# Kernel tuning notes

Hardware: AMD Instinct MI355X
Metric: run time of the kernel (lower is better)

The kernel has to match this reference:

```python
import jax, jax.numpy as jnp
import numpy as np

TIME_STEPS = 20
THRESHOLD = 1.0
DECAY = 0.9


def setup_inputs() -> dict:
    key = jax.random.key(0)
    x = jax.random.uniform(key, (64, 8192), dtype=jnp.float32)
    return {"x": x}


def reference(x):
    # LIF recurrence over TIME_STEPS: mem = decay*mem + x; spike = mem >= thr;
    # record (spike, mem); then mem -= spike*thr. Sequential -> lax.scan.
    thr = jnp.asarray(THRESHOLD, dtype=x.dtype)
    decay = jnp.asarray(DECAY, dtype=x.dtype)

    def step(mem, _):
        mem = decay * mem + x
        spikes = (mem >= thr).astype(x.dtype)
        mem_out = mem  # recorded before reset
        mem_next = mem - spikes * thr
        return mem_next, (spikes, mem_out)

    mem0 = jnp.zeros_like(x)
    _, (spike_trains, membrane_potentials) = jax.lax.scan(
        step, mem0, None, length=TIME_STEPS)
    # shapes: [T, batch, features]
    return spike_trains, membrane_potentials
```

## Files before the change

kernel.cpp:

```cpp
#include <hip/hip_runtime.h>


#define TSTEPS 20

typedef float v4f __attribute__((ext_vector_type(4)));

__global__ __launch_bounds__(256) void
TemporalEncoding_57672820850797_kernel(const v4f* __restrict__ x,
                                       float* __restrict__ out, int n4) {
    int i = blockIdx.x * blockDim.x + threadIdx.x;
    if (i >= n4) return;

    const v4f xv = __builtin_nontemporal_load(&x[i]);
    v4f* __restrict__ spikes = reinterpret_cast<v4f*>(out) + i;
    v4f* __restrict__ mems   = reinterpret_cast<v4f*>(out) + (size_t)TSTEPS * n4 + i;

    float m0 = 0.f, m1 = 0.f, m2 = 0.f, m3 = 0.f;

#pragma unroll
    for (int t = 0; t < TSTEPS; ++t) {
        m0 = __fadd_rn(__fmul_rn(0.9f, m0), xv.x);
        m1 = __fadd_rn(__fmul_rn(0.9f, m1), xv.y);
        m2 = __fadd_rn(__fmul_rn(0.9f, m2), xv.z);
        m3 = __fadd_rn(__fmul_rn(0.9f, m3), xv.w);

        float s0 = (m0 >= 1.0f) ? 1.0f : 0.0f;
        float s1 = (m1 >= 1.0f) ? 1.0f : 0.0f;
        float s2 = (m2 >= 1.0f) ? 1.0f : 0.0f;
        float s3 = (m3 >= 1.0f) ? 1.0f : 0.0f;

        v4f sv; sv.x = s0; sv.y = s1; sv.z = s2; sv.w = s3;
        v4f mv; mv.x = m0; mv.y = m1; mv.z = m2; mv.w = m3;
        __builtin_nontemporal_store(sv, spikes);
        __builtin_nontemporal_store(mv, mems);
        spikes += n4;
        mems   += n4;

        m0 -= s0;
        m1 -= s1;
        m2 -= s2;
        m3 -= s3;
    }
}

extern "C" void kernel_launch(void* const* d_in, const int* in_sizes, int n_in,
                              void* d_out, int out_size, void* d_ws, size_t ws_size,
                              hipStream_t stream) {
    const float* x = (const float*)d_in[0];
    float* out = (float*)d_out;
    const int n = in_sizes[0];
    const int n4 = n / 4;
    const int block = 256;
    const int grid = (n4 + block - 1) / block;
    TemporalEncoding_57672820850797_kernel<<<grid, block, 0, stream>>>(
        (const v4f*)x, out, n4);
}
```

Before: 90.29 us.

## Split output writes into contiguous per-block slabs with persistent grid-stride blocks

Replaces one-thread-per-element work (each thread writing 40 strided vectors across all time steps) with a persistent 512-block grid. Each work item covers one output type (spikes or membrane) and one group of 5 time steps, and recomputes the recurrence from zero up to that group. This makes each block write into one contiguous region of the output, which should improve DRAM write locality. The price is redundant recomputation of the recurrence and sizes hard-coded for this input shape. The load of x also changes from nontemporal to a normal load.

```diff
diff --git a/kernel.cpp b/kernel.cpp
--- a/kernel.cpp
+++ b/kernel.cpp
@@ -2,23 +2,19 @@
 
 
 #define TSTEPS 20
+#define TPER 5
+#define NGROUPS (TSTEPS / TPER)
+#define N4 131072
+#define CHUNKS 512
 
 typedef float v4f __attribute__((ext_vector_type(4)));
 
-__global__ __launch_bounds__(256) void
-TemporalEncoding_57672820850797_kernel(const v4f* __restrict__ x,
-                                       float* __restrict__ out, int n4) {
-    int i = blockIdx.x * blockDim.x + threadIdx.x;
-    if (i >= n4) return;
-
-    const v4f xv = __builtin_nontemporal_load(&x[i]);
-    v4f* __restrict__ spikes = reinterpret_cast<v4f*>(out) + i;
-    v4f* __restrict__ mems   = reinterpret_cast<v4f*>(out) + (size_t)TSTEPS * n4 + i;
-
+template <int TLO, bool SPIKES>
+__device__ __forceinline__ void run_store(const v4f xv, v4f* __restrict__ dst,
+                                          int n4) {
     float m0 = 0.f, m1 = 0.f, m2 = 0.f, m3 = 0.f;
-
 #pragma unroll
-    for (int t = 0; t < TSTEPS; ++t) {
+    for (int t = 0; t < TLO + TPER; ++t) {
         m0 = __fadd_rn(__fmul_rn(0.9f, m0), xv.x);
         m1 = __fadd_rn(__fmul_rn(0.9f, m1), xv.y);
         m2 = __fadd_rn(__fmul_rn(0.9f, m2), xv.z);
@@ -29,12 +25,12 @@
         float s2 = (m2 >= 1.0f) ? 1.0f : 0.0f;
         float s3 = (m3 >= 1.0f) ? 1.0f : 0.0f;
 
-        v4f sv; sv.x = s0; sv.y = s1; sv.z = s2; sv.w = s3;
-        v4f mv; mv.x = m0; mv.y = m1; mv.z = m2; mv.w = m3;
-        __builtin_nontemporal_store(sv, spikes);
-        __builtin_nontemporal_store(mv, mems);
-        spikes += n4;
-        mems   += n4;
+        if (t >= TLO) {
+            v4f v;
+            if (SPIKES) { v.x = s0; v.y = s1; v.z = s2; v.w = s3; }
+            else        { v.x = m0; v.y = m1; v.z = m2; v.w = m3; }
+            __builtin_nontemporal_store(v, dst + (size_t)(t - TLO) * n4);
+        }
 
         m0 -= s0;
         m1 -= s1;
@@ -43,15 +39,43 @@
     }
 }
 
+__global__ __launch_bounds__(256) void
+TemporalEncoding_57672820850797_kernel(const v4f* __restrict__ x,
+                                       float* __restrict__ out, int n4) {
+    v4f* out4 = reinterpret_cast<v4f*>(out);
+    const int total = 2 * NGROUPS * CHUNKS;
+
+    for (int w = blockIdx.x; w < total; w += gridDim.x) {
+        const int type  = w >> 11;
+        const int r     = w & 2047;
+        const int g     = r >> 9;
+        const int chunk = r & (CHUNKS - 1);
+        const int i     = chunk * 256 + threadIdx.x;
+
+        const v4f xv = x[i];
+
+        v4f* dst = out4 + (size_t)(type * TSTEPS + g * TPER) * n4 + i;
+        switch ((type << 2) | g) {
+            case 0: run_store< 0, true >(xv, dst, n4); break;
+            case 1: run_store< 5, true >(xv, dst, n4); break;
+            case 2: run_store<10, true >(xv, dst, n4); break;
+            case 3: run_store<15, true >(xv, dst, n4); break;
+            case 4: run_store< 0, false>(xv, dst, n4); break;
+            case 5: run_store< 5, false>(xv, dst, n4); break;
+            case 6: run_store<10, false>(xv, dst, n4); break;
+            case 7: run_store<15, false>(xv, dst, n4); break;
+        }
+    }
+}
+
 extern "C" void kernel_launch(void* const* d_in, const int* in_sizes, int n_in,
                               void* d_out, int out_size, void* d_ws, size_t ws_size,
                               hipStream_t stream) {
     const float* x = (const float*)d_in[0];
     float* out = (float*)d_out;
-    const int n = in_sizes[0];
-    const int n4 = n / 4;
+    const int n4 = in_sizes[0] / 4;
     const int block = 256;
-    const int grid = (n4 + block - 1) / block;
+    const int grid = 512;
     TemporalEncoding_57672820850797_kernel<<<grid, block, 0, stream>>>(
         (const v4f*)x, out, n4);
 }
```

After: 92.27 us. 2.2% more time.
